# Optimization experiments

Measured on AMD Instinct MI355X. Metric: run time of the kernel, lower is better.

Reference implementation:

```python
import jax, jax.numpy as jnp
import numpy as np

TEMPERATURE = 0.1
BASE_TEMPERATURE = 0.07
EPS = 1e-10


def setup_inputs() -> dict:
    key = jax.random.key(0)
    k1, k2 = jax.random.split(key)
    # feats_: [total_classes=64, n_view=128, feat_dim=256] sampled anchor features
    feats_ = jax.random.normal(k1, (64, 128, 256), dtype=jnp.float32)
    # labels_: class id per anchor group (21-class dataset -> repeats across groups)
    labels_ = jax.random.randint(k2, (64,), 0, 21, dtype=jnp.int32)
    return {"feats_": feats_, "labels_": labels_}


def reference(feats_, labels_):
    anchor_num, n_view, d = feats_.shape
    N = anchor_num * n_view
    # torch.cat(torch.unbind(feats_, dim=1), dim=0): view-major flattening
    cf = jnp.transpose(feats_, (1, 0, 2)).reshape(N, d)  # [N, d]
    # labels for the flattened ordering (mask.repeat tiles the [A,A] eq-mask)
    big_labels = jnp.tile(labels_, n_view)  # [N]

    logits = jnp.matmul(cf, cf.T) / TEMPERATURE  # [N, N]
    logits = logits - jax.lax.stop_gradient(jnp.max(logits, axis=1, keepdims=True))

    mask = (big_labels[:, None] == big_labels[None, :]).astype(jnp.float32)
    neg_mask = 1.0 - mask                       # negatives BEFORE removing diagonal
    mask = mask * (1.0 - jnp.eye(N, dtype=jnp.float32))  # positives exclude self

    exp_logits = jnp.exp(logits)
    neg_logits = jnp.sum(exp_logits * neg_mask, axis=1, keepdims=True)  # [N, 1]
    log_prob = logits - jnp.log(exp_logits + neg_logits + EPS)
    mean_log_prob_pos = jnp.sum(mask * log_prob, axis=1) / jnp.sum(mask, axis=1)
    loss = jnp.mean(-(TEMPERATURE / BASE_TEMPERATURE) * mean_log_prob_pos)
    return loss
```

## Files before the change

kernel.cpp:

```cpp
#include <hip/hip_runtime.h>
#include <hip/hip_bf16.h>

#define N_ROWS 8192
#define DIM 256
#define NANCH 64
#define NVIEW 128
#define NSTRIP 4
#define APS 16

typedef __attribute__((ext_vector_type(8))) short bf16x8;
typedef __attribute__((ext_vector_type(4))) float f32x4;
typedef __attribute__((ext_vector_type(4))) float float4v;
typedef __attribute__((ext_vector_type(4))) unsigned short ushort4v;

__device__ __forceinline__ unsigned short f2bf(float x) {
  union { float f; unsigned int u; } c; c.f = x;
  unsigned int u = c.u;
  unsigned int r = (u + 0x7fffu + ((u >> 16) & 1u)) >> 16;
  return (unsigned short)r;
}

__device__ __forceinline__ float bf2f(unsigned short b) {
  union { unsigned int u; float f; } c; c.u = ((unsigned int)b) << 16;
  return c.f;
}

__device__ __forceinline__ void gload_lds16(const void* g, void* l) {
  __builtin_amdgcn_global_load_lds(
      (const __attribute__((address_space(1))) unsigned int*)g,
      (__attribute__((address_space(3))) unsigned int*)l, 16, 0, 0);
}

__global__ void cast_diag_kernel(const float4v* __restrict__ in,
                                 ushort4v* __restrict__ out,
                                 float* __restrict__ diag) {
  const int w = threadIdx.x >> 6;
  const int l = threadIdx.x & 63;
  const int row = blockIdx.x * 4 + w;
  const float s = 3.16227766016838f;
  float4v v = in[row * 64 + l];
  ushort4v o;
  o.x = f2bf(v.x * s);
  o.y = f2bf(v.y * s);
  o.z = f2bf(v.z * s);
  o.w = f2bf(v.w * s);
  out[row * 64 + l] = o;
  float c0 = bf2f(o.x), c1 = bf2f(o.y), c2 = bf2f(o.z), c3 = bf2f(o.w);
  float ss = c0 * c0 + c1 * c1 + c2 * c2 + c3 * c3;
#pragma unroll
  for (int st = 1; st < 64; st <<= 1) ss += __shfl_xor(ss, st);
  if (l == 0) diag[row] = ss;
}

__global__ __launch_bounds__(1024, 4) void pcl_negsum(
    const unsigned short* __restrict__ Xb, const int* __restrict__ labels,
    const float* __restrict__ diag, float* __restrict__ ns_partial) {
  const int rb = blockIdx.x & 63;
  const int strip = blockIdx.x >> 6;
  const int tid = threadIdx.x;
  const int wid = tid >> 6;
  const int lane = tid & 63;
  const int lo = lane & 15;
  const int hi = lane >> 4;
  const int rg = wid >> 2;
  const int cg = wid & 3;

  __shared__ unsigned short buf[2][NVIEW * DIM];
  __shared__ float sns[16][32];
  __shared__ float sdiag[128];
  __shared__ int slab[NANCH];

  if (tid < NANCH) slab[tid] = labels[tid];
  if (tid >= 128 && tid < 256) sdiag[tid - 128] = diag[rb * 128 + tid - 128];
  __syncthreads();
  const int myLab = slab[rb];

  bf16x8 afrag[2][8];
#pragma unroll
  for (int ri = 0; ri < 2; ++ri) {
#pragma unroll
    for (int ks = 0; ks < 8; ++ks) {
      const unsigned short* p =
          Xb + (rb * 128 + rg * 32 + ri * 16 + lo) * DIM + ks * 32 + hi * 8;
      afrag[ri][ks] = *(const bf16x8*)p;
      asm volatile("" : "+v"(afrag[ri][ks]));
    }
  }

  float mreg[8], ns[8];
#pragma unroll
  for (int ri = 0; ri < 2; ++ri)
#pragma unroll
    for (int reg = 0; reg < 4; ++reg) {
      mreg[ri * 4 + reg] = sdiag[rg * 32 + ri * 16 + hi * 4 + reg];
      ns[ri * 4 + reg] = 0.f;
    }

  int srcoff[4];
#pragma unroll
  for (int i = 0; i < 4; ++i) {
    int g = i * 1024 + tid;
    int col = g >> 5, ch = g & 31;
    srcoff[i] = col * DIM + ((ch ^ (col & 7)) << 3);
  }
  const int ldsbase = (wid * 64) << 4;

  const unsigned short* astrip = Xb + (size_t)(strip * APS) * NVIEW * DIM;

#pragma unroll
  for (int i = 0; i < 4; ++i)
    gload_lds16(astrip + srcoff[i], (char*)&buf[0][0] + ldsbase + i * 16384);
  __syncthreads();

  const int x8 = lo & 7;
  int cb = 0;
  for (int a = 0; a < APS; ++a) {
    if (a + 1 < APS) {
      const unsigned short* src = astrip + (a + 1) * (NVIEW * DIM);
#pragma unroll
      for (int i = 0; i < 4; ++i)
        gload_lds16(src + srcoff[i], (char*)&buf[cb ^ 1][0] + ldsbase + i * 16384);
    }

    const bool isneg = (slab[strip * APS + a] != myLab);
    const char* bufc = (const char*)&buf[cb][0];
    f32x4 acc[2][2];
#pragma unroll
    for (int ri = 0; ri < 2; ++ri)
#pragma unroll
      for (int ci = 0; ci < 2; ++ci)
        acc[ri][ci] = (f32x4){0.f, 0.f, 0.f, 0.f};

#pragma unroll
    for (int ks = 0; ks < 8; ++ks) {
      const int sw = ((ks * 4 + hi) ^ x8) << 4;
      bf16x8 b0 = *(const bf16x8*)(bufc + (cg * 32 + lo) * 512 + sw);
      bf16x8 b1 = *(const bf16x8*)(bufc + (cg * 32 + 16 + lo) * 512 + sw);
      acc[0][0] = __builtin_amdgcn_mfma_f32_16x16x32_bf16(afrag[0][ks], b0, acc[0][0], 0, 0, 0);
      acc[0][1] = __builtin_amdgcn_mfma_f32_16x16x32_bf16(afrag[0][ks], b1, acc[0][1], 0, 0, 0);
      acc[1][0] = __builtin_amdgcn_mfma_f32_16x16x32_bf16(afrag[1][ks], b0, acc[1][0], 0, 0, 0);
      acc[1][1] = __builtin_amdgcn_mfma_f32_16x16x32_bf16(afrag[1][ks], b1, acc[1][1], 0, 0, 0);
    }

    if (isneg) {
#pragma unroll
      for (int ri = 0; ri < 2; ++ri)
#pragma unroll
        for (int reg = 0; reg < 4; ++reg) {
          const int t = ri * 4 + reg;
          float v0 = acc[ri][0][reg];
          float v1 = acc[ri][1][reg];
          if (__builtin_expect(fmaxf(v0, v1) > mreg[t] - 40.f, 0))
            ns[t] += __expf(v0 - mreg[t]) + __expf(v1 - mreg[t]);
        }
    }
    __syncthreads();
    cb ^= 1;
  }

#pragma unroll
  for (int t = 0; t < 8; ++t) {
#pragma unroll
    for (int st = 1; st < 16; st <<= 1) ns[t] += __shfl_xor(ns[t], st);
  }
  if (lo == 0) {
#pragma unroll
    for (int ri = 0; ri < 2; ++ri)
#pragma unroll
      for (int reg = 0; reg < 4; ++reg)
        sns[wid][ri * 16 + hi * 4 + reg] = ns[ri * 4 + reg];
  }
  __syncthreads();
  if (tid < 128) {
    const int rg2 = tid >> 5, r32 = tid & 31;
    float s = sns[rg2 * 4 + 0][r32] + sns[rg2 * 4 + 1][r32] +
              sns[rg2 * 4 + 2][r32] + sns[rg2 * 4 + 3][r32];
    ns_partial[strip * N_ROWS + rb * 128 + tid] = s;
  }
}

__global__ __launch_bounds__(1024, 4) void pcl_pos(
    const unsigned short* __restrict__ Xb, const int* __restrict__ labels,
    const float* __restrict__ diag, const float* __restrict__ ns_partial,
    float* __restrict__ partials) {
  const int blk = blockIdx.x;
  const int r0 = blk * 32;
  const int tid = threadIdx.x;
  const int wid = tid >> 6;
  const int lane = tid & 63;
  const int lo = lane & 15;
  const int hi = lane >> 4;
  const int cq = wid & 3;
  const int bq = wid >> 2;

  __shared__ int slab[NANCH];
  __shared__ float sred[16][32];
  __shared__ float smf[32];
  __shared__ float snsf[32];
  __shared__ int poslist[NANCH];
  __shared__ int scnt;

  if (tid < NANCH) slab[tid] = labels[tid];
  if (tid >= 64 && tid < 96) {
    int r = tid - 64;
    smf[r] = diag[r0 + r];
    snsf[r] = ns_partial[0 * N_ROWS + r0 + r] + ns_partial[1 * N_ROWS + r0 + r] +
              ns_partial[2 * N_ROWS + r0 + r] + ns_partial[3 * N_ROWS + r0 + r];
  }
  if (tid == 0) {
    int La0 = labels[blk >> 2];
    int c = 0;
    for (int b = 0; b < NANCH; ++b)
      if (labels[b] == La0) poslist[c++] = b;
    scnt = c;
  }
  __syncthreads();

  bf16x8 afrag[2][8];
#pragma unroll
  for (int ri = 0; ri < 2; ++ri) {
#pragma unroll
    for (int ks = 0; ks < 8; ++ks) {
      const unsigned short* p = Xb + (r0 + ri * 16 + lo) * DIM + ks * 32 + hi * 8;
      afrag[ri][ks] = *(const bf16x8*)p;
      asm volatile("" : "+v"(afrag[ri][ks]));
    }
  }

  const int cnt = scnt;
  float pos[8];
#pragma unroll
  for (int t = 0; t < 8; ++t) pos[t] = 0.f;

  for (int p = bq; p < cnt; p += 4) {
    const int b = poslist[p];
    const int c0 = b * NVIEW + cq * 32;
    f32x4 acc[2][2];
#pragma unroll
    for (int ri = 0; ri < 2; ++ri)
#pragma unroll
      for (int ci = 0; ci < 2; ++ci)
        acc[ri][ci] = (f32x4){0.f, 0.f, 0.f, 0.f};

#pragma unroll
    for (int ks = 0; ks < 8; ++ks) {
      bf16x8 b0 = *(const bf16x8*)(Xb + (c0 + lo) * DIM + ks * 32 + hi * 8);
      bf16x8 b1 = *(const bf16x8*)(Xb + (c0 + 16 + lo) * DIM + ks * 32 + hi * 8);
      acc[0][0] = __builtin_amdgcn_mfma_f32_16x16x32_bf16(afrag[0][ks], b0, acc[0][0], 0, 0, 0);
      acc[0][1] = __builtin_amdgcn_mfma_f32_16x16x32_bf16(afrag[0][ks], b1, acc[0][1], 0, 0, 0);
      acc[1][0] = __builtin_amdgcn_mfma_f32_16x16x32_bf16(afrag[1][ks], b0, acc[1][0], 0, 0, 0);
      acc[1][1] = __builtin_amdgcn_mfma_f32_16x16x32_bf16(afrag[1][ks], b1, acc[1][1], 0, 0, 0);
    }

#pragma unroll
    for (int ri = 0; ri < 2; ++ri) {
#pragma unroll
      for (int ci = 0; ci < 2; ++ci) {
#pragma unroll
        for (int reg = 0; reg < 4; ++reg) {
          const int t = ri * 4 + reg;
          const int row = ri * 16 + hi * 4 + reg;
          int grow = r0 + row;
          int gcol = c0 + ci * 16 + lo;
          if (grow != gcol) {
            float d = acc[ri][ci][reg] - smf[row];
            pos[t] += d - __logf(__expf(d) + snsf[row] + 1e-10f);
          }
        }
      }
    }
  }

#pragma unroll
  for (int t = 0; t < 8; ++t) {
#pragma unroll
    for (int st = 1; st < 16; st <<= 1) pos[t] += __shfl_xor(pos[t], st);
  }
  if (lo == 0) {
#pragma unroll
    for (int ri = 0; ri < 2; ++ri)
#pragma unroll
      for (int reg = 0; reg < 4; ++reg)
        sred[wid][ri * 16 + hi * 4 + reg] = pos[ri * 4 + reg];
  }
  __syncthreads();

  const float poscnt = (float)(cnt * NVIEW - 1);
  if (tid < 32) {
    float P = 0.f;
#pragma unroll
    for (int w = 0; w < 16; ++w) P += sred[w][tid];
    smf[tid] = P / poscnt;
  }
  __syncthreads();
  if (tid == 0) {
    float s = 0.f;
    for (int r = 0; r < 32; ++r) s += smf[r];
    partials[blk] = s;
  }
}

__global__ void final_reduce(const float* __restrict__ partials, float* __restrict__ out) {
  __shared__ float s[256];
  int t = threadIdx.x;
  s[t] = partials[t];
  __syncthreads();
  for (int st = 128; st > 0; st >>= 1) {
    if (t < st) s[t] += s[t + st];
    __syncthreads();
  }
  if (t == 0) out[0] = -(0.1f / 0.07f) * s[0] / (float)N_ROWS;
}

extern "C" void kernel_launch(void* const* d_in, const int* in_sizes, int n_in,
                              void* d_out, int out_size, void* d_ws, size_t ws_size,
                              hipStream_t stream) {
  const float* feats = (const float*)d_in[0];
  const int* labels = (const int*)d_in[1];
  float* out = (float*)d_out;

  unsigned short* Xb = (unsigned short*)d_ws;
  char* base = (char*)d_ws;
  float* diag = (float*)(base + (size_t)N_ROWS * DIM * 2);
  float* ns_partial = (float*)(base + (size_t)N_ROWS * DIM * 2 + N_ROWS * 4);
  float* partials = (float*)(base + (size_t)N_ROWS * DIM * 2 + N_ROWS * 4 +
                             NSTRIP * N_ROWS * 4);

  cast_diag_kernel<<<N_ROWS / 4, 256, 0, stream>>>((const float4v*)feats,
                                                   (ushort4v*)Xb, diag);
  pcl_negsum<<<NANCH * NSTRIP, 1024, 0, stream>>>(Xb, labels, diag, ns_partial);
  pcl_pos<<<N_ROWS / 32, 1024, 0, stream>>>(Xb, labels, diag, ns_partial, partials);
  final_reduce<<<1, 256, 0, stream>>>(partials, out);
}
```

Measured before the change: 79.31 us.

## Split negsum blocks into column halves with 512 threads for more blocks

The negative-sum kernel now splits each anchor's 128 views into two halves handled by separate 512-thread blocks. This doubles the grid to 512 blocks and halves the LDS double buffer per block. Partial sums grow from 4 to 8 per row, and the positive kernel sums all 8. The aim is better occupancy and load balance across CUs, at the cost of reloading the A fragments twice as often and writing more partials.

Measured after the change: 77.37 us. 1.03x faster.

```diff
diff --git a/kernel.cpp b/kernel.cpp
--- a/kernel.cpp
+++ b/kernel.cpp
@@ -7,6 +7,7 @@
 #define NVIEW 128
 #define NSTRIP 4
 #define APS 16
+#define NPART 8
 
 typedef __attribute__((ext_vector_type(8))) short bf16x8;
 typedef __attribute__((ext_vector_type(4))) float f32x4;
@@ -52,21 +53,23 @@
   if (l == 0) diag[row] = ss;
 }
 
-__global__ __launch_bounds__(1024, 4) void pcl_negsum(
+__global__ __launch_bounds__(512, 4) void pcl_negsum(
     const unsigned short* __restrict__ Xb, const int* __restrict__ labels,
     const float* __restrict__ diag, float* __restrict__ ns_partial) {
   const int rb = blockIdx.x & 63;
-  const int strip = blockIdx.x >> 6;
+  const int part = blockIdx.x >> 6;
+  const int strip = part >> 1;
+  const int half = part & 1;
   const int tid = threadIdx.x;
   const int wid = tid >> 6;
   const int lane = tid & 63;
   const int lo = lane & 15;
   const int hi = lane >> 4;
-  const int rg = wid >> 2;
-  const int cg = wid & 3;
-
-  __shared__ unsigned short buf[2][NVIEW * DIM];
-  __shared__ float sns[16][32];
+  const int rg = wid >> 1;
+  const int cg = wid & 1;
+
+  __shared__ unsigned short buf[2][64 * DIM];
+  __shared__ float sns[8][32];
   __shared__ float sdiag[128];
   __shared__ int slab[NANCH];
 
@@ -99,27 +102,28 @@
   int srcoff[4];
 #pragma unroll
   for (int i = 0; i < 4; ++i) {
-    int g = i * 1024 + tid;
+    int g = i * 512 + tid;
     int col = g >> 5, ch = g & 31;
     srcoff[i] = col * DIM + ((ch ^ (col & 7)) << 3);
   }
-  const int ldsbase = (wid * 64) << 4;
-
-  const unsigned short* astrip = Xb + (size_t)(strip * APS) * NVIEW * DIM;
+  const int ldsbase = wid * 1024;
+
+  const unsigned short* asrc0 =
+      Xb + ((size_t)(strip * APS) * NVIEW + half * 64) * DIM;
 
 #pragma unroll
   for (int i = 0; i < 4; ++i)
-    gload_lds16(astrip + srcoff[i], (char*)&buf[0][0] + ldsbase + i * 16384);
+    gload_lds16(asrc0 + srcoff[i], (char*)&buf[0][0] + ldsbase + i * 8192);
   __syncthreads();
 
   const int x8 = lo & 7;
   int cb = 0;
   for (int a = 0; a < APS; ++a) {
     if (a + 1 < APS) {
-      const unsigned short* src = astrip + (a + 1) * (NVIEW * DIM);
+      const unsigned short* src = asrc0 + (size_t)(a + 1) * NVIEW * DIM;
 #pragma unroll
       for (int i = 0; i < 4; ++i)
-        gload_lds16(src + srcoff[i], (char*)&buf[cb ^ 1][0] + ldsbase + i * 16384);
+        gload_lds16(src + srcoff[i], (char*)&buf[cb ^ 1][0] + ldsbase + i * 8192);
     }
 
     const bool isneg = (slab[strip * APS + a] != myLab);
@@ -173,9 +177,8 @@
   __syncthreads();
   if (tid < 128) {
     const int rg2 = tid >> 5, r32 = tid & 31;
-    float s = sns[rg2 * 4 + 0][r32] + sns[rg2 * 4 + 1][r32] +
-              sns[rg2 * 4 + 2][r32] + sns[rg2 * 4 + 3][r32];
-    ns_partial[strip * N_ROWS + rb * 128 + tid] = s;
+    float s = sns[rg2 * 2 + 0][r32] + sns[rg2 * 2 + 1][r32];
+    ns_partial[part * N_ROWS + rb * 128 + tid] = s;
   }
 }
 
@@ -204,8 +207,10 @@
   if (tid >= 64 && tid < 96) {
     int r = tid - 64;
     smf[r] = diag[r0 + r];
-    snsf[r] = ns_partial[0 * N_ROWS + r0 + r] + ns_partial[1 * N_ROWS + r0 + r] +
-              ns_partial[2 * N_ROWS + r0 + r] + ns_partial[3 * N_ROWS + r0 + r];
+    float s = 0.f;
+#pragma unroll
+    for (int p = 0; p < NPART; ++p) s += ns_partial[p * N_ROWS + r0 + r];
+    snsf[r] = s;
   }
   if (tid == 0) {
     int La0 = labels[blk >> 2];
@@ -319,16 +324,16 @@
   const int* labels = (const int*)d_in[1];
   float* out = (float*)d_out;
 
+  char* base = (char*)d_ws;
   unsigned short* Xb = (unsigned short*)d_ws;
-  char* base = (char*)d_ws;
   float* diag = (float*)(base + (size_t)N_ROWS * DIM * 2);
   float* ns_partial = (float*)(base + (size_t)N_ROWS * DIM * 2 + N_ROWS * 4);
   float* partials = (float*)(base + (size_t)N_ROWS * DIM * 2 + N_ROWS * 4 +
-                             NSTRIP * N_ROWS * 4);
+                             NPART * N_ROWS * 4);
 
   cast_diag_kernel<<<N_ROWS / 4, 256, 0, stream>>>((const float4v*)feats,
                                                    (ushort4v*)Xb, diag);
-  pcl_negsum<<<NANCH * NSTRIP, 1024, 0, stream>>>(Xb, labels, diag, ns_partial);
+  pcl_negsum<<<NANCH * NPART, 512, 0, stream>>>(Xb, labels, diag, ns_partial);
   pcl_pos<<<N_ROWS / 32, 1024, 0, stream>>>(Xb, labels, diag, ns_partial, partials);
   final_reduce<<<1, 256, 0, stream>>>(partials, out);
 }
```
